# Kernel tuning notes

Measured on AMD Instinct MI355X. Metric: run time of the kernel, lower is better.

Reference implementation:

```python
import jax, jax.numpy as jnp
import numpy as np

N_NODES = 100_000
N_EDGES = 1_600_000
F_IN = 128
HID = 64
C_OUT = 16


def setup_inputs() -> dict:
    key = jax.random.key(0)
    k1, k2, k3, k4, k5 = jax.random.split(key, 5)
    x = jax.random.normal(k1, (N_NODES, F_IN), dtype=jnp.float32)
    edge_index = jax.random.randint(k2, (2, N_EDGES), 0, N_NODES, dtype=jnp.int64)
    edge_weight = jax.random.uniform(k3, (N_EDGES,), dtype=jnp.float32)
    # Glorot-ish init for the two GCNConv linear layers; PyG inits bias to zero.
    W1 = jax.random.normal(k4, (F_IN, HID), dtype=jnp.float32) * (1.0 / np.sqrt(F_IN))
    b1 = jnp.zeros((HID,), dtype=jnp.float32)
    W2 = jax.random.normal(k5, (HID, C_OUT), dtype=jnp.float32) * (1.0 / np.sqrt(HID))
    b2 = jnp.zeros((C_OUT,), dtype=jnp.float32)
    return {"x": x, "edge_index": edge_index, "edge_weight": edge_weight,
            "W1": W1, "b1": b1, "W2": W2, "b2": b2}


def gcn_layer(x, row, col, ew, W, b, n):
    """PyG GCNConv: h = D^-1/2 (A + I) D^-1/2 (x W) + b, with edge weights.
    Self loops (weight 1) are handled analytically instead of appending edges."""
    h = x @ W  # [n, out]
    deg = jax.ops.segment_sum(ew, col, num_segments=n) + 1.0  # +1 for self loop
    dinv = jax.lax.rsqrt(deg)  # deg >= 1 always
    norm = dinv[row] * ew * dinv[col]  # [E]
    agg = jax.ops.segment_sum(norm[:, None] * h[row], col, num_segments=n)
    return agg + (dinv * dinv)[:, None] * h + b


def reference(x, edge_index, edge_weight, W1, b1, W2, b2):
    row, col = edge_index[0], edge_index[1]
    h = jax.nn.relu(gcn_layer(x, row, col, edge_weight, W1, b1, N_NODES))
    # delete_min_weighted_edges(node=0): remove the min-weight edge with source 0.
    # Zeroing its weight is mathematically identical to deleting it (it then
    # contributes 0 to both the degree and the aggregation).
    masked = jnp.where(row == 0, edge_weight, jnp.inf)
    idx = jnp.argmin(masked)
    ew2 = edge_weight.at[idx].set(0.0)
    return gcn_layer(h, row, col, ew2, W2, b2, N_NODES)
```

## Files before the change

### kernel.cpp

```cpp
#include <hip/hip_runtime.h>
#include <hip/hip_bf16.h>
#include <stdint.h>

#define NN 100000
#define NE 1600000
#define FIN 128
#define HID 64
#define COUT 16

#define BUKSH 8
#define BUKN 256
#define NBUK ((NN + BUKN - 1) >> BUKSH)
#define CAP 5120
#define PART_NB 200
#define EPB (NE / PART_NB)

typedef unsigned long long u64;
typedef short bf16x8 __attribute__((ext_vector_type(8)));
typedef float f32x4 __attribute__((ext_vector_type(4)));

struct Flags { int f32; int i64; };

__device__ __forceinline__ float b2f(__hip_bfloat16 v) { return __bfloat162float(v); }

__device__ __forceinline__ float ldf(const void* p, size_t i, int f32) {
    return f32 ? ((const float*)p)[i]
               : __bfloat162float(((const __hip_bfloat16*)p)[i]);
}
__device__ __forceinline__ int lde(const void* p, size_t i, int i64) {
    return i64 ? (int)((const long long*)p)[i] : ((const int*)p)[i];
}
__device__ __forceinline__ void ld4bf(const __hip_bfloat16* p, float& x0, float& x1,
                                      float& x2, float& x3) {
    union { uint2 u; __hip_bfloat16 h[4]; } v;
    v.u = *(const uint2*)p;
    x0 = b2f(v.h[0]); x1 = b2f(v.h[1]); x2 = b2f(v.h[2]); x3 = b2f(v.h[3]);
}
__device__ __forceinline__ unsigned short f2bfu(float f) {
    union { __hip_bfloat16 b; unsigned short u; } c;
    c.b = __float2bfloat16(f);
    return c.u;
}
__device__ __forceinline__ float bfu2f(unsigned short u) {
    union { unsigned short h[2]; float f; } c;
    c.h[0] = 0; c.h[1] = u;
    return c.f;
}

__global__ __launch_bounds__(256) void k_init(const unsigned short* xs,
                                              const int* ei32, Flags* fl,
                                              int* cursorA, u64* minkey,
                                              int* delpos) {
    int t = threadIdx.x;
    if (t < 64) {
        int lane = t;
        int huge = 0;
        for (int i = lane * 2; i < 1024; i += 128) {
            int e = (xs[i] >> 7) & 0xFF;
            if (e >= 0xC0) huge = 1;
        }
        int odd_nonzero = 0;
        for (int i = 1 + lane * 2; i < 512; i += 128) {
            if (ei32[i] != 0) odd_nonzero = 1;
        }
        u64 h = __ballot(huge), o = __ballot(odd_nonzero);
        if (lane == 0) { fl->f32 = (h != 0); fl->i64 = (o == 0); }
    }
    for (int i = t; i < NBUK; i += 256) cursorA[i] = 0;
    if (t == 64) *minkey = ~0ull;
    if (t == 65) *delpos = 0x7fffffff;
}

__global__ __launch_bounds__(256) void k_partA(const void* __restrict__ ei,
                                               const void* __restrict__ ew,
                                               const Flags* __restrict__ fl,
                                               int* __restrict__ cursorA,
                                               long long* __restrict__ tmp,
                                               u64* __restrict__ minkey) {
    __shared__ int cnt[NBUK];
    __shared__ int base[NBUK];
    __shared__ int colsh[EPB];
    int b = blockIdx.x, t = threadIdx.x;
    int f32 = fl->f32, i64 = fl->i64;
    for (int i = t; i < NBUK; i += 256) cnt[i] = 0;
    __syncthreads();
    int e0 = b * EPB;
    for (int i = t; i < EPB; i += 256) {
        int c = lde(ei, (size_t)NE + e0 + i, i64);
        colsh[i] = c;
        atomicAdd(&cnt[c >> BUKSH], 1);
    }
    __syncthreads();
    for (int i = t; i < NBUK; i += 256) {
        int n = cnt[i];
        base[i] = n ? atomicAdd(&cursorA[i], n) : 0;
    }
    __syncthreads();
    for (int i = t; i < NBUK; i += 256) cnt[i] = 0;
    __syncthreads();
    for (int i = t; i < EPB; i += 256) {
        int e = e0 + i;
        int r = lde(ei, e, i64);
        int c = colsh[i];
        float w = ldf(ew, e, f32);
        if (r == 0) {
            u64 key = ((u64)__float_as_uint(w) << 32) | (unsigned)e;
            atomicMin(minkey, key);
        }
        int buk = c >> BUKSH;
        int slot = base[buk] + atomicAdd(&cnt[buk], 1);
        if (slot < CAP) {
            unsigned lo = (unsigned)r | (((unsigned)c & 255u) << 17);
            tmp[(size_t)buk * CAP + slot] = ((long long)__float_as_int(w) << 32) | lo;
        }
    }
}

__global__ __launch_bounds__(256) void k_partB(const int* __restrict__ cursorA,
                                               const long long* __restrict__ tmp,
                                               int2* __restrict__ epack,
                                               int* __restrict__ rowptrN,
                                               const void* __restrict__ ei,
                                               const void* __restrict__ ew,
                                               const Flags* __restrict__ fl,
                                               const u64* __restrict__ minkey,
                                               float* __restrict__ dinv1,
                                               float* __restrict__ dinv2,
                                               int* __restrict__ delpos) {
    __shared__ long long tsl[CAP];
    __shared__ int cnt[256];
    __shared__ int pfx[256];
    __shared__ u64 wsum[256];
    int b = blockIdx.x, t = threadIdx.x;
    int count = cursorA[b]; if (count > CAP) count = CAP;
    const long long* ts = tmp + (size_t)b * CAP;
    for (int i = t; i < count; i += 256) tsl[i] = ts[i];
    int partial = 0;
    for (int i = t; i < NBUK; i += 256) {
        int cc = cursorA[i]; if (cc > CAP) cc = CAP;
        if (i < b) partial += cc;
    }
    pfx[t] = partial;
    __syncthreads();
    for (int off = 128; off > 0; off >>= 1) {
        if (t < off) pfx[t] += pfx[t + off];
        __syncthreads();
    }
    int gbase = pfx[0];
    __syncthreads();
    cnt[t] = 0; wsum[t] = 0;
    __syncthreads();
    if (b == NBUK - 1 && t == 0) rowptrN[NN] = gbase + count;
    u64 kk = *minkey;
    int eidx = (kk == ~0ull) ? 0 : (int)(kk & 0xffffffffu);
    int smin  = lde(ei, (size_t)eidx, fl->i64);
    int cmin  = lde(ei, (size_t)NE + eidx, fl->i64);
    int wminb = __float_as_int(ldf(ew, eidx, fl->f32));
    bool myb = (b == (cmin >> BUKSH));
    int clow = cmin & 255;
    for (int i = t; i < count; i += 256) {
        long long pk = tsl[i];
        unsigned lo = (unsigned)pk;
        int nl = (int)((lo >> 17) & 255u);
        atomicAdd(&cnt[nl], 1);
        float w = __int_as_float((int)(pk >> 32));
        atomicAdd(&wsum[nl], (u64)((double)w * 4294967296.0));
    }
    __syncthreads();
    int v = cnt[t];
    pfx[t] = v;
    for (int off = 1; off < 256; off <<= 1) {
        __syncthreads();
        int add = (t >= off) ? pfx[t - off] : 0;
        __syncthreads();
        pfx[t] += add;
    }
    __syncthreads();
    int excl = pfx[t] - v;
    int node = (b << BUKSH) + t;
    if (node < NN) {
        rowptrN[node] = gbase + excl;
        float degv = (float)((double)wsum[t] * (1.0 / 4294967296.0));
        float d1 = degv + 1.0f;
        float d2 = d1 - ((node == cmin) ? __int_as_float(wminb) : 0.0f);
        dinv1[node] = rsqrtf(d1);
        dinv2[node] = rsqrtf(d2);
    }
    __syncthreads();
    cnt[t] = gbase + excl;
    __syncthreads();
    for (int i = t; i < count; i += 256) {
        long long pk = tsl[i];
        unsigned lo = (unsigned)pk;
        int nl = (int)((lo >> 17) & 255u);
        int pos = atomicAdd(&cnt[nl], 1);
        long long outpk = (pk & 0xFFFFFFFF00000000LL) | (lo & 0x1FFFFu);
        *(long long*)(epack + pos) = outpk;
        if (myb && nl == clow && (int)(lo & 0x1FFFFu) == smin
            && (int)(pk >> 32) == wminb)
            atomicMin(delpos, pos);
    }
}

__global__ __launch_bounds__(256, 3) void k_gemm1(const void* __restrict__ xv_,
                                                  const void* __restrict__ W1_,
                                                  const Flags* __restrict__ fl,
                                                  const float* __restrict__ dinv1,
                                                  __hip_bfloat16* __restrict__ h1) {
    __shared__ __align__(16) unsigned short Wbuf[16384];
    int t = threadIdx.x;
    int wave = t >> 6, lane = t & 63;
    int quad = lane >> 4, col = lane & 15;
    if (fl->f32) {
        const float* x  = (const float*)xv_;
        const float* W1 = (const float*)W1_;
        unsigned short* Whi = Wbuf;
        unsigned short* Wlo = Wbuf + 8192;
        for (int i = t; i < 8192; i += 256) {
            int k = i >> 6;
            int n = i & 63;
            int kc = k >> 5, kr = k & 31;
            int q = kr >> 3, j = kr & 7;
            int n0 = n >> 4, c2 = n & 15;
            float w = W1[i];
            unsigned short hi = f2bfu(w);
            unsigned short lo = f2bfu(w - bfu2f(hi));
            int idx = ((n0 << 4) + (kc << 2) + q) * 128 + c2 * 8 + j;
            Whi[idx] = hi;
            Wlo[idx] = lo;
        }
        __syncthreads();
        bf16x8 Bh[4][4];
#pragma unroll
        for (int n0 = 0; n0 < 4; ++n0)
#pragma unroll
            for (int kc = 0; kc < 4; ++kc)
                Bh[kc][n0] = *(const bf16x8*)&Whi[((n0 << 4) + (kc << 2) + quad) * 128 + col * 8];
        int tile0 = (blockIdx.x * 4 + wave) * 2;
#pragma unroll 1
        for (int i = 0; i < 2; ++i) {
            int node0 = (tile0 + i) * 16;
            if (node0 >= NN) return;
            const float* xp = x + (size_t)(node0 + col) * FIN + quad * 8;
            float4 xv[8];
#pragma unroll
            for (int kc = 0; kc < 4; ++kc) {
                xv[2 * kc]     = *(const float4*)(xp + kc * 32);
                xv[2 * kc + 1] = *(const float4*)(xp + kc * 32 + 4);
            }
            f32x4 a0 = {0.f, 0.f, 0.f, 0.f}, a1 = a0, a2 = a0, a3 = a0;
#pragma unroll
            for (int kc = 0; kc < 4; ++kc) {
                float fv[8];
                fv[0] = xv[2 * kc].x;     fv[1] = xv[2 * kc].y;
                fv[2] = xv[2 * kc].z;     fv[3] = xv[2 * kc].w;
                fv[4] = xv[2 * kc + 1].x; fv[5] = xv[2 * kc + 1].y;
                fv[6] = xv[2 * kc + 1].z; fv[7] = xv[2 * kc + 1].w;
                bf16x8 Ah, Al;
#pragma unroll
                for (int j = 0; j < 8; ++j) {
                    unsigned short hi = f2bfu(fv[j]);
                    Ah[j] = (short)hi;
                    Al[j] = (short)f2bfu(fv[j] - bfu2f(hi));
                }
                int lbase = ((kc << 2) + quad) * 128 + col * 8;
                bf16x8 Bl0 = *(const bf16x8*)&Wlo[lbase];
                bf16x8 Bl1 = *(const bf16x8*)&Wlo[(1 << 4) * 128 + lbase];
                bf16x8 Bl2 = *(const bf16x8*)&Wlo[(2 << 4) * 128 + lbase];
                bf16x8 Bl3 = *(const bf16x8*)&Wlo[(3 << 4) * 128 + lbase];
                a0 = __builtin_amdgcn_mfma_f32_16x16x32_bf16(Ah, Bh[kc][0], a0, 0, 0, 0);
                a0 = __builtin_amdgcn_mfma_f32_16x16x32_bf16(Al, Bh[kc][0], a0, 0, 0, 0);
                a0 = __builtin_amdgcn_mfma_f32_16x16x32_bf16(Ah, Bl0,      a0, 0, 0, 0);
                a1 = __builtin_amdgcn_mfma_f32_16x16x32_bf16(Ah, Bh[kc][1], a1, 0, 0, 0);
                a1 = __builtin_amdgcn_mfma_f32_16x16x32_bf16(Al, Bh[kc][1], a1, 0, 0, 0);
                a1 = __builtin_amdgcn_mfma_f32_16x16x32_bf16(Ah, Bl1,      a1, 0, 0, 0);
                a2 = __builtin_amdgcn_mfma_f32_16x16x32_bf16(Ah, Bh[kc][2], a2, 0, 0, 0);
                a2 = __builtin_amdgcn_mfma_f32_16x16x32_bf16(Al, Bh[kc][2], a2, 0, 0, 0);
                a2 = __builtin_amdgcn_mfma_f32_16x16x32_bf16(Ah, Bl2,      a2, 0, 0, 0);
                a3 = __builtin_amdgcn_mfma_f32_16x16x32_bf16(Ah, Bh[kc][3], a3, 0, 0, 0);
                a3 = __builtin_amdgcn_mfma_f32_16x16x32_bf16(Al, Bh[kc][3], a3, 0, 0, 0);
                a3 = __builtin_amdgcn_mfma_f32_16x16x32_bf16(Ah, Bl3,      a3, 0, 0, 0);
            }
            __hip_bfloat16* hp = h1 + (size_t)(node0 + quad * 4) * HID + col;
#pragma unroll
            for (int r = 0; r < 4; ++r) {
                float dsc = dinv1[node0 + quad * 4 + r];
                hp[(size_t)r * HID + 0]  = __float2bfloat16(a0[r] * dsc);
                hp[(size_t)r * HID + 16] = __float2bfloat16(a1[r] * dsc);
                hp[(size_t)r * HID + 32] = __float2bfloat16(a2[r] * dsc);
                hp[(size_t)r * HID + 48] = __float2bfloat16(a3[r] * dsc);
            }
        }
    } else {
        const __hip_bfloat16* x = (const __hip_bfloat16*)xv_;
        const unsigned short* W1 = (const unsigned short*)W1_;
        unsigned short* Wf = Wbuf;
        for (int i = t; i < 8192; i += 256) {
            int k = i >> 6;
            int n = i & 63;
            int kc = k >> 5, kr = k & 31;
            int q = kr >> 3, j = kr & 7;
            int n0 = n >> 4, c2 = n & 15;
            Wf[((((n0 << 2) | kc) << 2) | q) * 128 + c2 * 8 + j] = W1[i];
        }
        __syncthreads();
        bf16x8 B[4][4];
#pragma unroll
        for (int n0 = 0; n0 < 4; ++n0)
#pragma unroll
            for (int kc = 0; kc < 4; ++kc)
                B[kc][n0] = *(const bf16x8*)&Wf[((((n0 << 2) | kc) << 2) | quad) * 128 + col * 8];
        int tile0 = (blockIdx.x * 4 + wave) * 2;
#pragma unroll 1
        for (int i = 0; i < 2; ++i) {
            int node0 = (tile0 + i) * 16;
            if (node0 >= NN) return;
            const __hip_bfloat16* xp = x + (size_t)(node0 + col) * FIN + quad * 8;
            f32x4 a0 = {0.f, 0.f, 0.f, 0.f}, a1 = a0, a2 = a0, a3 = a0;
#pragma unroll
            for (int kc = 0; kc < 4; ++kc) {
                bf16x8 A = *(const bf16x8*)(xp + kc * 32);
                a0 = __builtin_amdgcn_mfma_f32_16x16x32_bf16(A, B[kc][0], a0, 0, 0, 0);
                a1 = __builtin_amdgcn_mfma_f32_16x16x32_bf16(A, B[kc][1], a1, 0, 0, 0);
                a2 = __builtin_amdgcn_mfma_f32_16x16x32_bf16(A, B[kc][2], a2, 0, 0, 0);
                a3 = __builtin_amdgcn_mfma_f32_16x16x32_bf16(A, B[kc][3], a3, 0, 0, 0);
            }
            __hip_bfloat16* hp = h1 + (size_t)(node0 + quad * 4) * HID + col;
#pragma unroll
            for (int r = 0; r < 4; ++r) {
                float dsc = dinv1[node0 + quad * 4 + r];
                hp[(size_t)r * HID + 0]  = __float2bfloat16(a0[r] * dsc);
                hp[(size_t)r * HID + 16] = __float2bfloat16(a1[r] * dsc);
                hp[(size_t)r * HID + 32] = __float2bfloat16(a2[r] * dsc);
                hp[(size_t)r * HID + 48] = __float2bfloat16(a3[r] * dsc);
            }
        }
    }
}

__global__ __launch_bounds__(256) void k_agg1(const int* __restrict__ rowptrN,
                                              const int2* __restrict__ epack,
                                              const float* __restrict__ dinv1,
                                              const __hip_bfloat16* __restrict__ h1,
                                              const void* __restrict__ b1,
                                              const void* __restrict__ W2,
                                              const Flags* __restrict__ fl,
                                              const float* __restrict__ dinv2,
                                              float* __restrict__ h2) {
    __shared__ float Ws[HID * COUT];
    __shared__ float obuf[16][68];
    int t = threadIdx.x;
    int f32 = fl->f32;
    for (int i = t; i < HID * COUT; i += 256) Ws[i] = ldf(W2, i, f32);
    int nn = t >> 4;
    int n = blockIdx.x * 16 + nn;
    int l = t & 15;
    int f = l * 4;
    int wbase = t & 48;
    float dn = dinv1[n];
    int p0 = rowptrN[n], p1 = rowptrN[n + 1];
    float a0 = 0.f, a1 = 0.f, a2 = 0.f, a3 = 0.f;
    for (int p = p0; p < p1; p += 16) {
        int idx = p + l;
        int2 ev = make_int2(0, 0);
        if (idx < p1) ev = epack[idx];
        float cw = __int_as_float(ev.y);
        int rj[16];
#pragma unroll
        for (int j = 0; j < 16; ++j)
            rj[j] = __shfl(ev.x, wbase + j);
        uint2 raw[16];
#pragma unroll
        for (int j = 0; j < 16; ++j)
            raw[j] = *(const uint2*)(h1 + (size_t)rj[j] * HID + f);
#pragma unroll
        for (int j = 0; j < 16; ++j) {
            float c = __shfl(cw, wbase + j);
            union { uint2 u; __hip_bfloat16 h[4]; } v; v.u = raw[j];
            a0 += c * b2f(v.h[0]);
            a1 += c * b2f(v.h[1]);
            a2 += c * b2f(v.h[2]);
            a3 += c * b2f(v.h[3]);
        }
    }
    float x0, x1, x2, x3;
    ld4bf(h1 + (size_t)n * HID + f, x0, x1, x2, x3);
    obuf[nn][f + 0] = fmaxf(dn * (a0 + x0) + ldf(b1, f + 0, f32), 0.f);
    obuf[nn][f + 1] = fmaxf(dn * (a1 + x1) + ldf(b1, f + 1, f32), 0.f);
    obuf[nn][f + 2] = fmaxf(dn * (a2 + x2) + ldf(b1, f + 2, f32), 0.f);
    obuf[nn][f + 3] = fmaxf(dn * (a3 + x3) + ldf(b1, f + 3, f32), 0.f);
    __syncthreads();
    int c = t & 15;
    const float* orow = obuf[nn];
    float acc = 0.f;
#pragma unroll 8
    for (int k = 0; k < HID; ++k)
        acc += orow[k] * Ws[k * COUT + c];
    h2[(size_t)n * COUT + c] = acc * dinv2[n];
}

__global__ __launch_bounds__(256) void k_agg2(const int* __restrict__ rowptrN,
                                              const int2* __restrict__ epack,
                                              const float* __restrict__ dinv2,
                                              const float* __restrict__ h2,
                                              const void* __restrict__ bias2,
                                              const Flags* __restrict__ fl,
                                              const int* __restrict__ delpos,
                                              void* __restrict__ out) {
    int t = threadIdx.x;
    int n = blockIdx.x * 64 + (t >> 2);
    if (n >= NN) return;
    int l = t & 3;
    int f = l * 4;
    int wbase = t & 60;
    int f32 = fl->f32;
    int dp = *delpos;
    float dn = dinv2[n];
    int p0 = rowptrN[n], p1 = rowptrN[n + 1];
    float a0 = 0.f, a1 = 0.f, a2 = 0.f, a3 = 0.f;
    for (int p = p0; p < p1; p += 8) {
        int iA = p + l, iB = p + 4 + l;
        int2 evA = make_int2(0, 0), evB = make_int2(0, 0);
        if (iA < p1) evA = epack[iA];
        if (iB < p1) evB = epack[iB];
        float cwA = (iA == dp) ? 0.f : __int_as_float(evA.y);
        float cwB = (iB == dp) ? 0.f : __int_as_float(evB.y);
        int rj[8];
#pragma unroll
        for (int j = 0; j < 4; ++j) {
            rj[j]     = __shfl(evA.x, wbase + j);
            rj[4 + j] = __shfl(evB.x, wbase + j);
        }
        float4 hv[8];
#pragma unroll
        for (int j = 0; j < 8; ++j)
            hv[j] = *(const float4*)(h2 + (size_t)rj[j] * COUT + f);
#pragma unroll
        for (int j = 0; j < 4; ++j) {
            float cA = __shfl(cwA, wbase + j);
            float cB = __shfl(cwB, wbase + j);
            a0 += cA * hv[j].x + cB * hv[4 + j].x;
            a1 += cA * hv[j].y + cB * hv[4 + j].y;
            a2 += cA * hv[j].z + cB * hv[4 + j].z;
            a3 += cA * hv[j].w + cB * hv[4 + j].w;
        }
    }
    const float4 hn = *(const float4*)(h2 + (size_t)n * COUT + f);
    float o0 = dn * (a0 + hn.x) + ldf(bias2, f + 0, f32);
    float o1 = dn * (a1 + hn.y) + ldf(bias2, f + 1, f32);
    float o2 = dn * (a2 + hn.z) + ldf(bias2, f + 2, f32);
    float o3 = dn * (a3 + hn.w) + ldf(bias2, f + 3, f32);
    size_t idx = (size_t)n * COUT + f;
    if (f32) {
        float* op = (float*)out + idx;
        op[0] = o0; op[1] = o1; op[2] = o2; op[3] = o3;
    } else {
        union { uint2 u; __hip_bfloat16 h[4]; } pk;
        pk.h[0] = __float2bfloat16(o0); pk.h[1] = __float2bfloat16(o1);
        pk.h[2] = __float2bfloat16(o2); pk.h[3] = __float2bfloat16(o3);
        *(uint2*)((__hip_bfloat16*)out + idx) = pk.u;
    }
}

extern "C" void kernel_launch(void* const* d_in, const int* in_sizes, int n_in,
                              void* d_out, int out_size, void* d_ws, size_t ws_size,
                              hipStream_t stream) {
    const void* x  = d_in[0];
    const void* ei = d_in[1];
    const void* ew = d_in[2];
    const void* W1 = d_in[3];
    const void* b1 = d_in[4];
    const void* W2 = d_in[5];
    const void* b2 = d_in[6];

    char* wsb = (char*)d_ws;
    float* dinv1    = (float*)wsb;                     wsb += (size_t)NN * 4;
    float* dinv2    = (float*)wsb;                     wsb += (size_t)NN * 4;
    int*   rowptrN  = (int*)wsb;                       wsb += (size_t)(NN + 1) * 4;
    int*   cursorA  = (int*)wsb;                       wsb += (size_t)NBUK * 4;
    wsb = (char*)(((uintptr_t)wsb + 15) & ~(uintptr_t)15);
    int2*  epack    = (int2*)wsb;                      wsb += (size_t)NE * 8;
    __hip_bfloat16* h1 = (__hip_bfloat16*)wsb;         wsb += (size_t)NN * HID * 2;
    float* h2       = (float*)wsb;                     wsb += (size_t)NN * COUT * 4;
    long long* tmp  = (long long*)wsb;                 wsb += (size_t)NBUK * CAP * 8;
    u64*   minkey   = (u64*)wsb;                       wsb += 8;
    Flags* fl       = (Flags*)wsb;                     wsb += 8;
    int*   delpos   = (int*)wsb;                       wsb += 8;

    k_init<<<1, 256, 0, stream>>>((const unsigned short*)x, (const int*)ei, fl,
                                  cursorA, minkey, delpos);
    k_partA<<<PART_NB, 256, 0, stream>>>(ei, ew, fl, cursorA, tmp, minkey);
    k_partB<<<NBUK, 256, 0, stream>>>(cursorA, tmp, epack, rowptrN,
                                      ei, ew, fl, minkey, dinv1, dinv2, delpos);
    k_gemm1<<<(NN / 16 + 7) / 8, 256, 0, stream>>>(x, W1, fl, dinv1, h1);
    k_agg1<<<NN / 16, 256, 0, stream>>>(rowptrN, epack, dinv1, h1, b1, W2, fl,
                                        dinv2, h2);
    k_agg2<<<(NN + 63) / 64, 256, 0, stream>>>(rowptrN, epack, dinv2, h2, b2, fl,
                                               delpos, d_out);
}
```

Measured before the change: 257.2 us.

## Replace two-pass bucket partition with global atomic counting-sort CSR build

The old bucketed partition (shared-memory histograms, a fixed-capacity tmp buffer, a per-bucket local sort) is replaced by a straightforward counting sort. Per-node global atomics count degree and weight sums, a two-kernel scan builds rowptr, and a scatter pass places edges with per-node atomic cursors. This drops the tmp staging buffer and the CAP overflow risk, at the cost of many global atomics on 100k counters and an extra full read of the edge arrays. Edge order within a row becomes nondeterministic, and delpos is now taken directly from the min-edge index.

```diff
diff --git a/kernel.cpp b/kernel.cpp
--- a/kernel.cpp
+++ b/kernel.cpp
@@ -9,11 +9,7 @@
 #define COUT 16
 
 #define BUKSH 8
-#define BUKN 256
-#define NBUK ((NN + BUKN - 1) >> BUKSH)
-#define CAP 5120
-#define PART_NB 200
-#define EPB (NE / PART_NB)
+#define NBUK ((NN + 255) >> BUKSH)
 
 typedef unsigned long long u64;
 typedef short bf16x8 __attribute__((ext_vector_type(8)));
@@ -47,99 +43,76 @@
     return c.f;
 }
 
-__global__ __launch_bounds__(256) void k_init(const unsigned short* xs,
-                                              const int* ei32, Flags* fl,
-                                              int* cursorA, u64* minkey,
-                                              int* delpos) {
-    int t = threadIdx.x;
-    if (t < 64) {
-        int lane = t;
-        int huge = 0;
-        for (int i = lane * 2; i < 1024; i += 128) {
-            int e = (xs[i] >> 7) & 0xFF;
-            if (e >= 0xC0) huge = 1;
-        }
-        int odd_nonzero = 0;
-        for (int i = 1 + lane * 2; i < 512; i += 128) {
-            if (ei32[i] != 0) odd_nonzero = 1;
-        }
-        u64 h = __ballot(huge), o = __ballot(odd_nonzero);
-        if (lane == 0) { fl->f32 = (h != 0); fl->i64 = (o == 0); }
-    }
-    for (int i = t; i < NBUK; i += 256) cursorA[i] = 0;
-    if (t == 64) *minkey = ~0ull;
-    if (t == 65) *delpos = 0x7fffffff;
-}
-
-__global__ __launch_bounds__(256) void k_partA(const void* __restrict__ ei,
+__global__ __launch_bounds__(64) void k_init(const unsigned short* xs,
+                                             const int* ei32, Flags* fl,
+                                             u64* minkey, int* delpos) {
+    int lane = threadIdx.x;
+    int huge = 0;
+    for (int i = lane * 2; i < 1024; i += 128) {
+        int e = (xs[i] >> 7) & 0xFF;
+        if (e >= 0xC0) huge = 1;
+    }
+    int odd_nonzero = 0;
+    for (int i = 1 + lane * 2; i < 512; i += 128) {
+        if (ei32[i] != 0) odd_nonzero = 1;
+    }
+    u64 h = __ballot(huge), o = __ballot(odd_nonzero);
+    if (lane == 0) {
+        fl->f32 = (h != 0); fl->i64 = (o == 0);
+        *minkey = ~0ull;
+        *delpos = 0;
+    }
+}
+
+__global__ __launch_bounds__(256) void k_count(const void* __restrict__ ei,
                                                const void* __restrict__ ew,
                                                const Flags* __restrict__ fl,
-                                               int* __restrict__ cursorA,
-                                               long long* __restrict__ tmp,
+                                               int* __restrict__ cnt,
+                                               u64* __restrict__ wsum,
                                                u64* __restrict__ minkey) {
-    __shared__ int cnt[NBUK];
-    __shared__ int base[NBUK];
-    __shared__ int colsh[EPB];
+    int e = blockIdx.x * 256 + threadIdx.x;
+    if (e >= NE) return;
+    int i64 = fl->i64, f32 = fl->f32;
+    int c = lde(ei, (size_t)NE + e, i64);
+    float w = ldf(ew, e, f32);
+    atomicAdd(&cnt[c], 1);
+    atomicAdd(&wsum[c], (u64)((double)w * 4294967296.0));
+    int r = lde(ei, e, i64);
+    if (r == 0) {
+        u64 key = ((u64)__float_as_uint(w) << 32) | (unsigned)e;
+        atomicMin(minkey, key);
+    }
+}
+
+__global__ __launch_bounds__(256) void k_s1(const int* __restrict__ cnt,
+                                            int* __restrict__ bsum) {
+    __shared__ int sm[256];
     int b = blockIdx.x, t = threadIdx.x;
-    int f32 = fl->f32, i64 = fl->i64;
-    for (int i = t; i < NBUK; i += 256) cnt[i] = 0;
+    int node = (b << 8) + t;
+    sm[t] = (node < NN) ? cnt[node] : 0;
     __syncthreads();
-    int e0 = b * EPB;
-    for (int i = t; i < EPB; i += 256) {
-        int c = lde(ei, (size_t)NE + e0 + i, i64);
-        colsh[i] = c;
-        atomicAdd(&cnt[c >> BUKSH], 1);
-    }
-    __syncthreads();
-    for (int i = t; i < NBUK; i += 256) {
-        int n = cnt[i];
-        base[i] = n ? atomicAdd(&cursorA[i], n) : 0;
-    }
-    __syncthreads();
-    for (int i = t; i < NBUK; i += 256) cnt[i] = 0;
-    __syncthreads();
-    for (int i = t; i < EPB; i += 256) {
-        int e = e0 + i;
-        int r = lde(ei, e, i64);
-        int c = colsh[i];
-        float w = ldf(ew, e, f32);
-        if (r == 0) {
-            u64 key = ((u64)__float_as_uint(w) << 32) | (unsigned)e;
-            atomicMin(minkey, key);
-        }
-        int buk = c >> BUKSH;
-        int slot = base[buk] + atomicAdd(&cnt[buk], 1);
-        if (slot < CAP) {
-            unsigned lo = (unsigned)r | (((unsigned)c & 255u) << 17);
-            tmp[(size_t)buk * CAP + slot] = ((long long)__float_as_int(w) << 32) | lo;
-        }
-    }
-}
-
-__global__ __launch_bounds__(256) void k_partB(const int* __restrict__ cursorA,
-                                               const long long* __restrict__ tmp,
-                                               int2* __restrict__ epack,
-                                               int* __restrict__ rowptrN,
-                                               const void* __restrict__ ei,
-                                               const void* __restrict__ ew,
-                                               const Flags* __restrict__ fl,
-                                               const u64* __restrict__ minkey,
-                                               float* __restrict__ dinv1,
-                                               float* __restrict__ dinv2,
-                                               int* __restrict__ delpos) {
-    __shared__ long long tsl[CAP];
-    __shared__ int cnt[256];
+    for (int off = 128; off > 0; off >>= 1) {
+        if (t < off) sm[t] += sm[t + off];
+        __syncthreads();
+    }
+    if (t == 0) bsum[b] = sm[0];
+}
+
+__global__ __launch_bounds__(256) void k_s2(const int* __restrict__ cnt,
+                                            const int* __restrict__ bsum,
+                                            const u64* __restrict__ wsum,
+                                            const void* __restrict__ ei,
+                                            const void* __restrict__ ew,
+                                            const Flags* __restrict__ fl,
+                                            const u64* __restrict__ minkey,
+                                            int* __restrict__ rowptrN,
+                                            float* __restrict__ dinv1,
+                                            float* __restrict__ dinv2) {
     __shared__ int pfx[256];
-    __shared__ u64 wsum[256];
     int b = blockIdx.x, t = threadIdx.x;
-    int count = cursorA[b]; if (count > CAP) count = CAP;
-    const long long* ts = tmp + (size_t)b * CAP;
-    for (int i = t; i < count; i += 256) tsl[i] = ts[i];
     int partial = 0;
-    for (int i = t; i < NBUK; i += 256) {
-        int cc = cursorA[i]; if (cc > CAP) cc = CAP;
-        if (i < b) partial += cc;
-    }
+    for (int i = t; i < NBUK; i += 256)
+        if (i < b) partial += bsum[i];
     pfx[t] = partial;
     __syncthreads();
     for (int off = 128; off > 0; off >>= 1) {
@@ -148,58 +121,52 @@
     }
     int gbase = pfx[0];
     __syncthreads();
-    cnt[t] = 0; wsum[t] = 0;
+    int node = (b << 8) + t;
+    int v = (node < NN) ? cnt[node] : 0;
+    pfx[t] = v;
+    for (int off = 1; off < 256; off <<= 1) {
+        __syncthreads();
+        int add = (t >= off) ? pfx[t - off] : 0;
+        __syncthreads();
+        pfx[t] += add;
+    }
     __syncthreads();
-    if (b == NBUK - 1 && t == 0) rowptrN[NN] = gbase + count;
+    int excl = pfx[t] - v;
+    if (node < NN) {
+        rowptrN[node] = gbase + excl;
+        float degv = (float)((double)wsum[node] * (1.0 / 4294967296.0));
+        u64 kk = *minkey;
+        int eidx = (kk == ~0ull) ? 0 : (int)(kk & 0xffffffffu);
+        int cmin = lde(ei, (size_t)NE + eidx, fl->i64);
+        float wmin = ldf(ew, eidx, fl->f32);
+        float d1 = degv + 1.0f;
+        float d2 = d1 - ((node == cmin) ? wmin : 0.0f);
+        dinv1[node] = rsqrtf(d1);
+        dinv2[node] = rsqrtf(d2);
+    }
+    if (b == NBUK - 1 && t == 255) rowptrN[NN] = gbase + pfx[255];
+}
+
+__global__ __launch_bounds__(256) void k_place(const void* __restrict__ ei,
+                                               const void* __restrict__ ew,
+                                               const Flags* __restrict__ fl,
+                                               const int* __restrict__ rowptrN,
+                                               int* __restrict__ cursor,
+                                               const u64* __restrict__ minkey,
+                                               int2* __restrict__ epack,
+                                               int* __restrict__ delpos) {
+    int e = blockIdx.x * 256 + threadIdx.x;
+    if (e >= NE) return;
+    int i64 = fl->i64, f32 = fl->f32;
+    int c = lde(ei, (size_t)NE + e, i64);
+    int r = lde(ei, e, i64);
+    float w = ldf(ew, e, f32);
+    int pos = rowptrN[c] + atomicAdd(&cursor[c], 1);
+    int2 ev; ev.x = r; ev.y = __float_as_int(w);
+    epack[pos] = ev;
     u64 kk = *minkey;
     int eidx = (kk == ~0ull) ? 0 : (int)(kk & 0xffffffffu);
-    int smin  = lde(ei, (size_t)eidx, fl->i64);
-    int cmin  = lde(ei, (size_t)NE + eidx, fl->i64);
-    int wminb = __float_as_int(ldf(ew, eidx, fl->f32));
-    bool myb = (b == (cmin >> BUKSH));
-    int clow = cmin & 255;
-    for (int i = t; i < count; i += 256) {
-        long long pk = tsl[i];
-        unsigned lo = (unsigned)pk;
-        int nl = (int)((lo >> 17) & 255u);
-        atomicAdd(&cnt[nl], 1);
-        float w = __int_as_float((int)(pk >> 32));
-        atomicAdd(&wsum[nl], (u64)((double)w * 4294967296.0));
-    }
-    __syncthreads();
-    int v = cnt[t];
-    pfx[t] = v;
-    for (int off = 1; off < 256; off <<= 1) {
-        __syncthreads();
-        int add = (t >= off) ? pfx[t - off] : 0;
-        __syncthreads();
-        pfx[t] += add;
-    }
-    __syncthreads();
-    int excl = pfx[t] - v;
-    int node = (b << BUKSH) + t;
-    if (node < NN) {
-        rowptrN[node] = gbase + excl;
-        float degv = (float)((double)wsum[t] * (1.0 / 4294967296.0));
-        float d1 = degv + 1.0f;
-        float d2 = d1 - ((node == cmin) ? __int_as_float(wminb) : 0.0f);
-        dinv1[node] = rsqrtf(d1);
-        dinv2[node] = rsqrtf(d2);
-    }
-    __syncthreads();
-    cnt[t] = gbase + excl;
-    __syncthreads();
-    for (int i = t; i < count; i += 256) {
-        long long pk = tsl[i];
-        unsigned lo = (unsigned)pk;
-        int nl = (int)((lo >> 17) & 255u);
-        int pos = atomicAdd(&cnt[nl], 1);
-        long long outpk = (pk & 0xFFFFFFFF00000000LL) | (lo & 0x1FFFFu);
-        *(long long*)(epack + pos) = outpk;
-        if (myb && nl == clow && (int)(lo & 0x1FFFFu) == smin
-            && (int)(pk >> 32) == wminb)
-            atomicMin(delpos, pos);
-    }
+    if (e == eidx) *delpos = pos;
 }
 
 __global__ __launch_bounds__(256, 3) void k_gemm1(const void* __restrict__ xv_,
@@ -474,24 +441,32 @@
     const void* b2 = d_in[6];
 
     char* wsb = (char*)d_ws;
+    char* zbase = wsb;
+    int*   cnt      = (int*)wsb;                       wsb += (size_t)NN * 4;
+    int*   cursor   = (int*)wsb;                       wsb += (size_t)NN * 4;
+    u64*   wsum     = (u64*)wsb;                       wsb += (size_t)NN * 8;
+    size_t zbytes = (size_t)wsb - (size_t)zbase;
     float* dinv1    = (float*)wsb;                     wsb += (size_t)NN * 4;
     float* dinv2    = (float*)wsb;                     wsb += (size_t)NN * 4;
     int*   rowptrN  = (int*)wsb;                       wsb += (size_t)(NN + 1) * 4;
-    int*   cursorA  = (int*)wsb;                       wsb += (size_t)NBUK * 4;
+    int*   bsum     = (int*)wsb;                       wsb += (size_t)NBUK * 4;
     wsb = (char*)(((uintptr_t)wsb + 15) & ~(uintptr_t)15);
     int2*  epack    = (int2*)wsb;                      wsb += (size_t)NE * 8;
     __hip_bfloat16* h1 = (__hip_bfloat16*)wsb;         wsb += (size_t)NN * HID * 2;
     float* h2       = (float*)wsb;                     wsb += (size_t)NN * COUT * 4;
-    long long* tmp  = (long long*)wsb;                 wsb += (size_t)NBUK * CAP * 8;
     u64*   minkey   = (u64*)wsb;                       wsb += 8;
     Flags* fl       = (Flags*)wsb;                     wsb += 8;
     int*   delpos   = (int*)wsb;                       wsb += 8;
 
-    k_init<<<1, 256, 0, stream>>>((const unsigned short*)x, (const int*)ei, fl,
-                                  cursorA, minkey, delpos);
-    k_partA<<<PART_NB, 256, 0, stream>>>(ei, ew, fl, cursorA, tmp, minkey);
-    k_partB<<<NBUK, 256, 0, stream>>>(cursorA, tmp, epack, rowptrN,
-                                      ei, ew, fl, minkey, dinv1, dinv2, delpos);
+    hipMemsetAsync(zbase, 0, zbytes, stream);
+    k_init<<<1, 64, 0, stream>>>((const unsigned short*)x, (const int*)ei, fl,
+                                 minkey, delpos);
+    k_count<<<(NE + 255) / 256, 256, 0, stream>>>(ei, ew, fl, cnt, wsum, minkey);
+    k_s1<<<NBUK, 256, 0, stream>>>(cnt, bsum);
+    k_s2<<<NBUK, 256, 0, stream>>>(cnt, bsum, wsum, ei, ew, fl, minkey,
+                                   rowptrN, dinv1, dinv2);
+    k_place<<<(NE + 255) / 256, 256, 0, stream>>>(ei, ew, fl, rowptrN, cursor,
+                                                  minkey, epack, delpos);
     k_gemm1<<<(NN / 16 + 7) / 8, 256, 0, stream>>>(x, W1, fl, dinv1, h1);
     k_agg1<<<NN / 16, 256, 0, stream>>>(rowptrN, epack, dinv1, h1, b1, W2, fl,
                                         dinv2, h2);
```

After: 430.4 us. 1.67x slower.
